# Kernel tuning notes

Measured on AMD Instinct MI355X. Metric: run time of the kernel, lower is better.

## Reference

```python
import jax, jax.numpy as jnp
import numpy as np

M, N, H, K1, K2, C, B = 100000, 14000, 256, 16, 32, 7, 64
EPS = 1e-8


def setup_inputs() -> dict:
    key = jax.random.key(0)
    ks = jax.random.split(key, 8)
    embeds = jax.random.normal(ks[0], (M, H), dtype=jnp.float32)
    idx = jax.random.randint(ks[1], (N,), 0, M, dtype=jnp.int32)
    neighbors = jax.random.randint(ks[2], (N, K1), 0, M, dtype=jnp.int32)
    neighbors_2hop = jax.random.randint(ks[3], (N, K2), 0, M, dtype=jnp.int32)
    labels = (jnp.arange(N, dtype=jnp.int32) % C)  # perfectly balanced, as averageemb requires
    # prompt params (downstreamprompt weights, xavier-uniform [1,H])
    lim = float(np.sqrt(6.0 / (1 + H)))
    w_self = jax.random.uniform(ks[4], (1, H), jnp.float32, -lim, lim)
    w_n = jax.random.uniform(ks[5], (1, H), jnp.float32, -lim, lim)
    w_n2 = jax.random.uniform(ks[6], (1, H), jnp.float32, -lim, lim)
    # metanet (PromptVector): bottleneck adapter H -> B -> H
    k7, k8 = jax.random.split(ks[7])
    W1 = jax.random.normal(k7, (H, B), jnp.float32) * (1.0 / np.sqrt(H))
    b1 = jnp.zeros((B,), jnp.float32)
    W2 = jax.random.normal(k8, (B, H), jnp.float32) * (1.0 / np.sqrt(B))
    b2 = jnp.zeros((H,), jnp.float32)
    return {"embeds": embeds, "w_self": w_self, "w_n": w_n, "w_n2": w_n2,
            "W1": W1, "b1": b1, "W2": W2, "b2": b2,
            "idx": idx, "neighbors": neighbors, "neighbors_2hop": neighbors_2hop,
            "labels": labels}


def _cos(a, b):
    # torch.cosine_similarity with eps=1e-8 (clamped norms)
    num = jnp.sum(a * b, axis=-1)
    na = jnp.maximum(jnp.sqrt(jnp.sum(a * a, axis=-1)), EPS)
    nb = jnp.maximum(jnp.sqrt(jnp.sum(b * b, axis=-1)), EPS)
    return num / (na * nb)


def reference(embeds, w_self, w_n, w_n2, W1, b1, W2, b2,
              idx, neighbors, neighbors_2hop, labels):
    center = embeds[idx]                         # [N,H]
    ce = w_self * center                         # selfprompt: [N,H]
    nb = jnp.nan_to_num(w_n * embeds[neighbors])              # [N,K1,H]
    nb2 = jnp.nan_to_num(w_n2 * embeds[neighbors_2hop])       # [N,K2,H]
    nb_all = jnp.concatenate([nb, nb2], axis=1)  # [N,K1+K2,H]
    sim = _cos(ce[:, None, :], nb_all)           # [N,K]
    w = jax.nn.softmax(sim, axis=-1)
    weighted_neighbors = jnp.einsum('nk,nkh->nh', w, nb_all)
    inputs = weighted_neighbors + ce             # (dropout = identity at eval)
    prompts = jax.nn.elu(inputs @ W1 + b1) @ W2 + b2  # metanet adapter
    rawret = prompts + ce                        # [N,H]
    # averageemb: per-class mean (labels balanced, N/C per class)
    per_class = N // C
    ave = jax.ops.segment_sum(rawret, labels, num_segments=C) / per_class  # [C,H]
    ret = jax.nn.softmax(_cos(rawret[:, None, :], ave[None, :, :]), axis=1)  # [N,C]
    return ret
```

## Files before the change

kernel.cpp:

```cpp
#include <hip/hip_runtime.h>
#include <hip/hip_bf16.h>
#include <math.h>

#define H 256
#define NR 14000
#define MR 100000
#define K1C 16
#define K2C 32
#define KT 48
#define CC 7
#define EPSF 1e-8f
#define GP 448
#define CH2 32

typedef __attribute__((ext_vector_type(8))) unsigned short ushort8_t;

__device__ __forceinline__ float rdlane(float v, int l) {
    return __int_as_float(__builtin_amdgcn_readlane(__float_as_int(v), l));
}

__device__ __forceinline__ float dot4(const float4 a, const float4 b) {
    return a.x * b.x + a.y * b.y + a.z * b.z + a.w * b.w;
}

__device__ __forceinline__ unsigned short f2bf(float x) {
    __hip_bfloat16 h = __float2bfloat16(x);
    return *(unsigned short*)&h;
}

__global__ __launch_bounds__(256) void kE(const float* __restrict__ src,
                                          unsigned short* __restrict__ dst) {
    const size_t base = ((size_t)blockIdx.x * 256 + threadIdx.x) * 8;
    const float4 a = *(const float4*)(src + base);
    const float4 b = *(const float4*)(src + base + 4);
    ushort8_t o;
    o[0] = f2bf(a.x); o[1] = f2bf(a.y); o[2] = f2bf(a.z); o[3] = f2bf(a.w);
    o[4] = f2bf(b.x); o[5] = f2bf(b.y); o[6] = f2bf(b.z); o[7] = f2bf(b.w);
    *(ushort8_t*)(dst + base) = o;
}

__global__ __launch_bounds__(256, 2) void kA4(
    const float* __restrict__ embeds, const unsigned short* __restrict__ ebf,
    const float* __restrict__ w_self, const float* __restrict__ w_n,
    const float* __restrict__ w_n2, const int* __restrict__ idx,
    const int* __restrict__ nbr1, const int* __restrict__ nbr2,
    float* __restrict__ inbuf, float* __restrict__ cebuf)
{
    const int tid = threadIdx.x;
    const int wv = tid >> 6, lane = tid & 63;
    const int n = blockIdx.x * 4 + wv;
    const int g = lane >> 4, l = lane & 15;
    const int hb = l * 16;

    const int cidx = idx[n];
    int ridx = 0;
    if (lane < K1C) ridx = nbr1[n * K1C + lane];
    else if (lane < KT) ridx = nbr2[n * K2C + (lane - K1C)];

    const float* crow = embeds + (size_t)cidx * H + hb;
    float4 cv4[4], wsv4[4], wnv4[4], wn2v4[4];
#pragma unroll
    for (int j = 0; j < 4; ++j) {
        cv4[j]   = *(const float4*)(crow + 4 * j);
        wsv4[j]  = *(const float4*)(w_self + hb + 4 * j);
        wnv4[j]  = *(const float4*)(w_n    + hb + 4 * j);
        wn2v4[j] = *(const float4*)(w_n2   + hb + 4 * j);
    }

    int rows[12];
#pragma unroll
    for (int kk = 0; kk < 12; ++kk) rows[kk] = __shfl(ridx, kk * 4 + g);
    ushort8_t pb[24];
#pragma unroll
    for (int kk = 0; kk < 12; ++kk) {
        const unsigned short* rp = ebf + (size_t)rows[kk] * H + hb;
        pb[2 * kk]     = *(const ushort8_t*)(rp);
        pb[2 * kk + 1] = *(const ushort8_t*)(rp + 8);
    }

    float ce[16], wn[16], wn2[16];
    float na2 = 0.f;
#pragma unroll
    for (int j = 0; j < 4; ++j) {
        wn[4*j+0] = wnv4[j].x;  wn[4*j+1] = wnv4[j].y;
        wn[4*j+2] = wnv4[j].z;  wn[4*j+3] = wnv4[j].w;
        wn2[4*j+0] = wn2v4[j].x; wn2[4*j+1] = wn2v4[j].y;
        wn2[4*j+2] = wn2v4[j].z; wn2[4*j+3] = wn2v4[j].w;
        ce[4*j+0] = wsv4[j].x * cv4[j].x; ce[4*j+1] = wsv4[j].y * cv4[j].y;
        ce[4*j+2] = wsv4[j].z * cv4[j].z; ce[4*j+3] = wsv4[j].w * cv4[j].w;
        na2 += ce[4*j+0]*ce[4*j+0] + ce[4*j+1]*ce[4*j+1]
             + ce[4*j+2]*ce[4*j+2] + ce[4*j+3]*ce[4*j+3];
    }
#pragma unroll
    for (int m = 1; m <= 8; m <<= 1) na2 += __shfl_xor(na2, m);
    const float na = fmaxf(sqrtf(na2), EPSF);

    float acc[16];
#pragma unroll
    for (int i = 0; i < 16; ++i) acc[i] = 0.f;
    float lsum = 0.f;

#pragma unroll
    for (int kk = 0; kk < 12; ++kk) {
        const ushort8_t e0 = pb[2 * kk];
        const ushort8_t e1 = pb[2 * kk + 1];
        float nb[16];
#pragma unroll
        for (int i = 0; i < 8; ++i) {
            nb[i]     = __uint_as_float((unsigned)e0[i] << 16);
            nb[8 + i] = __uint_as_float((unsigned)e1[i] << 16);
        }
        float num = 0.f, nn = 0.f;
#pragma unroll
        for (int i = 0; i < 16; ++i) {
            const float w = (kk < 4) ? wn[i] : wn2[i];
            nb[i] *= w;
            num += ce[i] * nb[i];
            nn  += nb[i] * nb[i];
        }
#pragma unroll
        for (int m = 1; m <= 8; m <<= 1) {
            num += __shfl_xor(num, m);
            nn  += __shfl_xor(nn, m);
        }
        const float nbn = fmaxf(sqrtf(nn), EPSF);
        const float e = __expf(num / (nbn * na) - 1.0f);
        lsum += e;
#pragma unroll
        for (int i = 0; i < 16; ++i) acc[i] += e * nb[i];
    }
#pragma unroll
    for (int m = 16; m <= 32; m <<= 1) {
        lsum += __shfl_xor(lsum, m);
#pragma unroll
        for (int i = 0; i < 16; ++i) acc[i] += __shfl_xor(acc[i], m);
    }
    const float rl = 1.0f / lsum;
    if (g == 0) {
        float* ip = inbuf + (size_t)n * H + hb;
        float* cp = cebuf + (size_t)n * H + hb;
#pragma unroll
        for (int i = 0; i < 16; ++i) {
            ip[i] = acc[i] * rl + ce[i];
            cp[i] = ce[i];
        }
    }
}

__global__ __launch_bounds__(256) void kB2(
    float* __restrict__ io, const float* __restrict__ cebuf,
    const float* __restrict__ W1, const float* __restrict__ b1,
    const float* __restrict__ W2, const float* __restrict__ b2)
{
    const int tid = threadIdx.x;
    const int wv = tid >> 6, lane = tid & 63;
    const int r0 = __builtin_amdgcn_readfirstlane((blockIdx.x * 4 + wv) * 4);
    const float* inb = io + (size_t)r0 * H;

    float hid[4];
    const float bb = b1[lane];
#pragma unroll
    for (int r = 0; r < 4; ++r) hid[r] = bb;

#pragma unroll 8
    for (int h = 0; h < 256; ++h) {
        const float w1v = W1[h * 64 + lane];
        hid[0] += inb[h]           * w1v;
        hid[1] += inb[H + h]       * w1v;
        hid[2] += inb[2 * H + h]   * w1v;
        hid[3] += inb[3 * H + h]   * w1v;
    }
#pragma unroll
    for (int r = 0; r < 4; ++r)
        hid[r] = hid[r] > 0.f ? hid[r] : (__expf(hid[r]) - 1.0f);

    float4 p4[4];
    const float4 b2v = *(const float4*)(b2 + 4 * lane);
#pragma unroll
    for (int r = 0; r < 4; ++r) p4[r] = b2v;
#pragma unroll 4
    for (int b = 0; b < 64; ++b) {
        const float4 w2v = *(const float4*)(W2 + b * H + 4 * lane);
#pragma unroll
        for (int r = 0; r < 4; ++r) {
            const float hv = rdlane(hid[r], b);
            p4[r].x += hv * w2v.x; p4[r].y += hv * w2v.y;
            p4[r].z += hv * w2v.z; p4[r].w += hv * w2v.w;
        }
    }
#pragma unroll
    for (int r = 0; r < 4; ++r) {
        const float4 cev = *(const float4*)(cebuf + (size_t)(r0 + r) * H + 4 * lane);
        float4 ov;
        ov.x = p4[r].x + cev.x; ov.y = p4[r].y + cev.y;
        ov.z = p4[r].z + cev.z; ov.w = p4[r].w + cev.w;
        *(float4*)(io + (size_t)(r0 + r) * H + 4 * lane) = ov;
    }
}

__global__ __launch_bounds__(256) void kC1(
    const float* __restrict__ rawret, const int* __restrict__ labels,
    float* __restrict__ partial)
{
    const int t = threadIdx.x, j = blockIdx.x;
    const int nlo = j * CH2;
    const int nhi = min(nlo + CH2, NR);
    float acc[CC];
#pragma unroll
    for (int c = 0; c < CC; ++c) acc[c] = 0.f;
    for (int n = nlo; n < nhi; n += 4) {
        int lab[4]; float v[4];
#pragma unroll
        for (int u = 0; u < 4; ++u) {
            lab[u] = labels[n + u];
            v[u] = rawret[(size_t)(n + u) * H + t];
        }
#pragma unroll
        for (int u = 0; u < 4; ++u)
#pragma unroll
            for (int c = 0; c < CC; ++c) acc[c] += (lab[u] == c) ? v[u] : 0.f;
    }
#pragma unroll
    for (int c = 0; c < CC; ++c) partial[(size_t)(j * CC + c) * H + t] = acc[c];
}

__global__ __launch_bounds__(256) void kC2(
    const float* __restrict__ partial, float* __restrict__ ave)
{
    const int b = blockIdx.x, c = b >> 3, s = b & 7;
    const int hloc = threadIdx.x & 31, jg = threadIdx.x >> 5;
    const int h = 32 * s + hloc;
    float sum = 0.f;
#pragma unroll 8
    for (int j = jg; j < GP; j += 8)
        sum += partial[(size_t)(j * CC + c) * H + h];
    __shared__ float red[256];
    red[threadIdx.x] = sum;
    __syncthreads();
    if (jg == 0) {
#pragma unroll
        for (int t = 1; t < 8; ++t) sum += red[t * 32 + hloc];
        ave[c * H + h] = sum * (1.0f / 2000.0f);
    }
}

__global__ __launch_bounds__(256) void kD2(
    const float* __restrict__ rawret, const float* __restrict__ ave,
    float* __restrict__ out)
{
    const int tid = threadIdx.x;
    const int wv = tid >> 6, lane = tid & 63;
    const int n = blockIdx.x * 4 + wv;
    const float4 r4 = *(const float4*)(rawret + (size_t)n * H + 4 * lane);
    float nr2 = dot4(r4, r4);
#pragma unroll
    for (int m = 1; m <= 32; m <<= 1) nr2 += __shfl_xor(nr2, m);
    const float rn = fmaxf(sqrtf(nr2), EPSF);

    float e[CC];
    float s = 0.f;
#pragma unroll
    for (int c = 0; c < CC; ++c) {
        const float4 a4 = *(const float4*)(ave + c * H + 4 * lane);
        float d = dot4(r4, a4);
        float an = dot4(a4, a4);
#pragma unroll
        for (int m = 1; m <= 32; m <<= 1) {
            d  += __shfl_xor(d, m);
            an += __shfl_xor(an, m);
        }
        const float anorm = fmaxf(sqrtf(an), EPSF);
        const float sim = d / (rn * anorm);
        e[c] = __expf(sim - 1.0f);
        s += e[c];
    }
    const float rs = 1.0f / s;
    if (lane < CC) {
        float v = e[0];
#pragma unroll
        for (int c = 1; c < CC; ++c) v = (lane == c) ? e[c] : v;
        out[(size_t)n * CC + lane] = v * rs;
    }
}

extern "C" void kernel_launch(void* const* d_in, const int* in_sizes, int n_in,
                              void* d_out, int out_size, void* d_ws, size_t ws_size,
                              hipStream_t stream) {
    const float* embeds = (const float*)d_in[0];
    const float* w_self = (const float*)d_in[1];
    const float* w_n    = (const float*)d_in[2];
    const float* w_n2   = (const float*)d_in[3];
    const float* W1     = (const float*)d_in[4];
    const float* b1     = (const float*)d_in[5];
    const float* W2     = (const float*)d_in[6];
    const float* b2     = (const float*)d_in[7];
    const int* idx      = (const int*)d_in[8];
    const int* nbr1     = (const int*)d_in[9];
    const int* nbr2     = (const int*)d_in[10];
    const int* labels   = (const int*)d_in[11];
    float* out = (float*)d_out;

    float* rawret  = (float*)d_ws;
    float* cebuf   = rawret + (size_t)NR * H;
    float* partial = cebuf + (size_t)NR * H;
    float* ave     = partial + (size_t)GP * CC * H;
    unsigned short* ebf = (unsigned short*)(ave + CC * H + 8);

    kE<<<(MR * H) / (256 * 8), 256, 0, stream>>>(embeds, ebf);
    kA4<<<NR / 4, 256, 0, stream>>>(embeds, ebf, w_self, w_n, w_n2,
                                    idx, nbr1, nbr2, rawret, cebuf);
    kB2<<<NR / 16, 256, 0, stream>>>(rawret, cebuf, W1, b1, W2, b2);
    kC1<<<GP, 256, 0, stream>>>(rawret, labels, partial);
    kC2<<<56, 256, 0, stream>>>(partial, ave);
    kD2<<<NR / 4, 256, 0, stream>>>(rawret, ave, out);
}
```

Before: 308.7 us.

## Fuse metanet adapter MLP into the neighbor-attention gather kernel

Folds the H->64->H bottleneck adapter into the per-node attention kernel, so each wave computes the hidden layer with readlane broadcasts and the output layer split across its four lane groups, then reduces with shuffles. This removes the intermediate inbuf/cebuf global writes and re-reads, plus one kernel launch. In exchange, each node now re-reads W1 and W2 (served from cache), there are more per-wave shuffles, and register pressure rises in a kernel already bounded to 2 blocks per SM.

```diff
diff --git a/kernel.cpp b/kernel.cpp
--- a/kernel.cpp
+++ b/kernel.cpp
@@ -39,12 +39,14 @@
     *(ushort8_t*)(dst + base) = o;
 }
 
-__global__ __launch_bounds__(256, 2) void kA4(
+__global__ __launch_bounds__(256, 2) void kA5(
     const float* __restrict__ embeds, const unsigned short* __restrict__ ebf,
     const float* __restrict__ w_self, const float* __restrict__ w_n,
     const float* __restrict__ w_n2, const int* __restrict__ idx,
     const int* __restrict__ nbr1, const int* __restrict__ nbr2,
-    float* __restrict__ inbuf, float* __restrict__ cebuf)
+    const float* __restrict__ W1, const float* __restrict__ b1,
+    const float* __restrict__ W2, const float* __restrict__ b2,
+    float* __restrict__ rawret)
 {
     const int tid = threadIdx.x;
     const int wv = tid >> 6, lane = tid & 63;
@@ -136,65 +138,57 @@
         for (int i = 0; i < 16; ++i) acc[i] += __shfl_xor(acc[i], m);
     }
     const float rl = 1.0f / lsum;
+    float inv[16];
+#pragma unroll
+    for (int i = 0; i < 16; ++i) inv[i] = acc[i] * rl + ce[i];
+
+    float hid = b1[lane];
+    const float* w1p = W1 + lane;
+#pragma unroll
+    for (int l2 = 0; l2 < 16; ++l2) {
+#pragma unroll
+        for (int i = 0; i < 16; ++i) {
+            const int h = 16 * l2 + i;
+            hid = fmaf(rdlane(inv[i], l2), w1p[h * 64], hid);
+        }
+    }
+    hid = hid > 0.f ? hid : (__expf(hid) - 1.0f);
+
+    float p[16];
+#pragma unroll
+    for (int i = 0; i < 16; ++i) p[i] = 0.f;
+    const int gb = lane & 48;
+#pragma unroll
+    for (int t = 0; t < 16; ++t) {
+        const float hv = __shfl(hid, gb + t);
+        const float* w2p = W2 + (size_t)(gb + t) * H + hb;
+#pragma unroll
+        for (int j = 0; j < 4; ++j) {
+            const float4 w2v = *(const float4*)(w2p + 4 * j);
+            p[4*j+0] = fmaf(hv, w2v.x, p[4*j+0]);
+            p[4*j+1] = fmaf(hv, w2v.y, p[4*j+1]);
+            p[4*j+2] = fmaf(hv, w2v.z, p[4*j+2]);
+            p[4*j+3] = fmaf(hv, w2v.w, p[4*j+3]);
+        }
+    }
+#pragma unroll
+    for (int m = 16; m <= 32; m <<= 1) {
+#pragma unroll
+        for (int i = 0; i < 16; ++i) p[i] += __shfl_xor(p[i], m);
+    }
+
     if (g == 0) {
-        float* ip = inbuf + (size_t)n * H + hb;
-        float* cp = cebuf + (size_t)n * H + hb;
-#pragma unroll
-        for (int i = 0; i < 16; ++i) {
-            ip[i] = acc[i] * rl + ce[i];
-            cp[i] = ce[i];
-        }
-    }
-}
-
-__global__ __launch_bounds__(256) void kB2(
-    float* __restrict__ io, const float* __restrict__ cebuf,
-    const float* __restrict__ W1, const float* __restrict__ b1,
-    const float* __restrict__ W2, const float* __restrict__ b2)
-{
-    const int tid = threadIdx.x;
-    const int wv = tid >> 6, lane = tid & 63;
-    const int r0 = __builtin_amdgcn_readfirstlane((blockIdx.x * 4 + wv) * 4);
-    const float* inb = io + (size_t)r0 * H;
-
-    float hid[4];
-    const float bb = b1[lane];
-#pragma unroll
-    for (int r = 0; r < 4; ++r) hid[r] = bb;
-
-#pragma unroll 8
-    for (int h = 0; h < 256; ++h) {
-        const float w1v = W1[h * 64 + lane];
-        hid[0] += inb[h]           * w1v;
-        hid[1] += inb[H + h]       * w1v;
-        hid[2] += inb[2 * H + h]   * w1v;
-        hid[3] += inb[3 * H + h]   * w1v;
-    }
-#pragma unroll
-    for (int r = 0; r < 4; ++r)
-        hid[r] = hid[r] > 0.f ? hid[r] : (__expf(hid[r]) - 1.0f);
-
-    float4 p4[4];
-    const float4 b2v = *(const float4*)(b2 + 4 * lane);
-#pragma unroll
-    for (int r = 0; r < 4; ++r) p4[r] = b2v;
-#pragma unroll 4
-    for (int b = 0; b < 64; ++b) {
-        const float4 w2v = *(const float4*)(W2 + b * H + 4 * lane);
-#pragma unroll
-        for (int r = 0; r < 4; ++r) {
-            const float hv = rdlane(hid[r], b);
-            p4[r].x += hv * w2v.x; p4[r].y += hv * w2v.y;
-            p4[r].z += hv * w2v.z; p4[r].w += hv * w2v.w;
-        }
-    }
-#pragma unroll
-    for (int r = 0; r < 4; ++r) {
-        const float4 cev = *(const float4*)(cebuf + (size_t)(r0 + r) * H + 4 * lane);
-        float4 ov;
-        ov.x = p4[r].x + cev.x; ov.y = p4[r].y + cev.y;
-        ov.z = p4[r].z + cev.z; ov.w = p4[r].w + cev.w;
-        *(float4*)(io + (size_t)(r0 + r) * H + 4 * lane) = ov;
+        float* op = rawret + (size_t)n * H + hb;
+#pragma unroll
+        for (int j = 0; j < 4; ++j) {
+            const float4 b2v = *(const float4*)(b2 + hb + 4 * j);
+            float4 ov;
+            ov.x = p[4*j+0] + b2v.x + ce[4*j+0];
+            ov.y = p[4*j+1] + b2v.y + ce[4*j+1];
+            ov.z = p[4*j+2] + b2v.z + ce[4*j+2];
+            ov.w = p[4*j+3] + b2v.w + ce[4*j+3];
+            *(float4*)(op + 4 * j) = ov;
+        }
     }
 }
 
@@ -301,15 +295,13 @@
     float* out = (float*)d_out;
 
     float* rawret  = (float*)d_ws;
-    float* cebuf   = rawret + (size_t)NR * H;
-    float* partial = cebuf + (size_t)NR * H;
+    float* partial = rawret + (size_t)NR * H;
     float* ave     = partial + (size_t)GP * CC * H;
     unsigned short* ebf = (unsigned short*)(ave + CC * H + 8);
 
     kE<<<(MR * H) / (256 * 8), 256, 0, stream>>>(embeds, ebf);
-    kA4<<<NR / 4, 256, 0, stream>>>(embeds, ebf, w_self, w_n, w_n2,
-                                    idx, nbr1, nbr2, rawret, cebuf);
-    kB2<<<NR / 16, 256, 0, stream>>>(rawret, cebuf, W1, b1, W2, b2);
+    kA5<<<NR / 4, 256, 0, stream>>>(embeds, ebf, w_self, w_n, w_n2,
+                                    idx, nbr1, nbr2, W1, b1, W2, b2, rawret);
     kC1<<<GP, 256, 0, stream>>>(rawret, labels, partial);
     kC2<<<56, 256, 0, stream>>>(partial, ave);
     kD2<<<NR / 4, 256, 0, stream>>>(rawret, ave, out);
```

New measurement: 343.3 us. 11.2% more time.
